# Kernel tuning notes

Hardware: AMD Instinct MI355X
Metric: run time of the kernel (lower is better)

Reference implementation:

```python
import jax, jax.numpy as jnp
import numpy as np

B, L, D = 4, 4096, 1024
H = 4
DK = D // H          # head key dim = 256
DV = D // H          # head value dim = 256
CHUNK = 32
CONV_K = 4
FIR_S, FIR_L = 5, 63
N_PATHS = 4
TAU_MIN = 0.25
HARD_FLOOR = 0.005
LEARN_FLOOR_MAX = 0.07
EPS = 1e-5


def _silu(x):
    return x * jax.nn.sigmoid(x)


def _l2norm(x):
    return x * jax.lax.rsqrt(jnp.sum(x * x, -1, keepdims=True) + 1e-6)


def _causal_dw_conv(x, filt):
    # x: (B, L, C); filt: (C, K). Depthwise causal conv1d.
    C, K = filt.shape
    xp = jnp.pad(x, ((0, 0), (K - 1, 0), (0, 0)))
    w = filt.T[:, None, :]  # (K, 1, C)
    return jax.lax.conv_general_dilated(xp, w, (1,), 'VALID',
                                        dimension_numbers=('NWC', 'WIO', 'NWC'),
                                        feature_group_count=C)


def _fir(x, filt):
    # x: (B, L, H, Dv); filt: (H, Dv, K)
    b, l, h, d = x.shape
    y = _causal_dw_conv(x.reshape(b, l, h * d), filt.reshape(h * d, filt.shape[-1]))
    return y.reshape(b, l, h, d)


def _delta_rule_chunkwise(q, k, v, beta):
    # q,k: (B,H,L,dk); v: (B,H,L,dv); beta: (B,H,L). L must be a multiple of CHUNK.
    b, h, Lq, dk = q.shape
    dv = v.shape[-1]
    q = _l2norm(q)
    k = _l2norm(k)
    v = v * beta[..., None]
    kb = k * beta[..., None]
    n = Lq // CHUNK
    r = lambda t: t.reshape(b, h, n, CHUNK, t.shape[-1])
    q, k, v, kb = r(q), r(k), r(v), r(kb)
    # A = strictly-lower part of -(k_beta @ k^T); the torch row loop computes
    # (I - A)^{-1} - I via forward substitution, then adds I back.
    A = -jnp.einsum('bhnid,bhnjd->bhnij', kb, k)
    A = jnp.tril(A, -1)
    eye = jnp.eye(CHUNK, dtype=q.dtype)
    Tinv = jax.scipy.linalg.solve_triangular(eye - A, jnp.broadcast_to(eye, A.shape),
                                             lower=True, unit_diagonal=True)
    u = Tinv @ v   # (b,h,n,c,dv)
    w = Tinv @ kb  # (b,h,n,c,dk)

    def step(S, inp):
        q_i, k_i, u_i, w_i = inp  # (b,h,c,d)
        attn = jnp.tril(jnp.einsum('bhid,bhjd->bhij', q_i, k_i))  # incl. diagonal
        u_adj = u_i - w_i @ S
        o_i = q_i @ S + attn @ u_adj
        S_new = S + jnp.einsum('bhcd,bhce->bhde', k_i, u_adj)
        return S_new, o_i

    S0 = jnp.zeros((b, h, dk, dv), dtype=q.dtype)
    xs = tuple(jnp.moveaxis(t, 2, 0) for t in (q, k, u, w))
    S, o = jax.lax.scan(step, S0, xs)
    o = jnp.moveaxis(o, 0, 2).reshape(b, h, Lq, dv)
    return o, S


def _stats(p):
    # p: (B,L,H,D) -> (B,L,H*4): mean, var (biased), mean|.|, l2 norm
    mean = p.mean(-1)
    var = p.var(-1)
    absm = jnp.abs(p).mean(-1)
    l2 = jnp.sqrt(jnp.sum(p * p, -1))
    s = jnp.stack([mean, var, absm, l2], -1)
    return s.reshape(p.shape[0], p.shape[1], -1)


def setup_inputs() -> dict:
    key = jax.random.key(0)
    ks = jax.random.split(key, 16)
    rn = lambda i, shape, s=0.02: jax.random.normal(ks[i], shape, jnp.float32) * s
    GATE_IN = D + 16 * H
    GATE_H = D * 2 // 2
    return {
        'hidden_states': jax.random.normal(ks[0], (B, L, D), jnp.float32),
        'Wq': rn(1, (D, D)), 'Wk': rn(2, (D, D)), 'Wv': rn(3, (D, D)),
        'Wb': rn(4, (H, D)),
        'conv_q_w': rn(5, (D, CONV_K), 0.2),
        'conv_k_w': rn(6, (D, CONV_K), 0.2),
        'conv_v_w': rn(7, (D, CONV_K), 0.2),
        'fir_short_w': rn(8, (H, DV, FIR_S)).at[..., -1].add(1.0),
        'fir_long_w': rn(9, (H, DV, FIR_L)).at[..., -1].add(1.0),
        'log_temp': jnp.zeros((H, N_PATHS), jnp.float32),
        'floor_param': jnp.full((H, N_PATHS), -2.0, jnp.float32),
        'gate_W1': rn(10, (GATE_H, GATE_IN)),
        'gate_b1': jnp.zeros((GATE_H,), jnp.float32),
        'gate_W2': rn(11, (H * N_PATHS, GATE_H)),
        'gate_b2': jnp.zeros((H * N_PATHS,), jnp.float32).at[N_PATHS - 1::N_PATHS].set(2.0),
        'o_norm_w': jnp.ones((DV,), jnp.float32),
        'Wo': rn(12, (D, D)),
    }


def reference(hidden_states, Wq, Wk, Wv, Wb, conv_q_w, conv_k_w, conv_v_w,
              fir_short_w, fir_long_w, log_temp, floor_param,
              gate_W1, gate_b1, gate_W2, gate_b2, o_norm_w, Wo):
    b, l, _ = hidden_states.shape
    # projections + short depthwise causal conv with silu activation
    q = _silu(_causal_dw_conv(hidden_states @ Wq.T, conv_q_w))
    k = _silu(_causal_dw_conv(hidden_states @ Wk.T, conv_k_w))
    v = _silu(_causal_dw_conv(hidden_states @ Wv.T, conv_v_w))
    beta = jax.nn.sigmoid(hidden_states @ Wb.T)  # (b,l,H)

    q_h = q.reshape(b, l, H, DK).transpose(0, 2, 1, 3)
    k_h = k.reshape(b, l, H, DK).transpose(0, 2, 1, 3)
    v_h = v.reshape(b, l, H, DV).transpose(0, 2, 1, 3)
    o_d, _S = _delta_rule_chunkwise(q_h, k_h, v_h, beta.transpose(0, 2, 1))
    path_delta = o_d.transpose(0, 2, 1, 3)  # (b,l,H,DV)

    v_direct = v.reshape(b, l, H, DV)
    path_short = _fir(v_direct, fir_short_w)
    path_long = _fir(v_direct, fir_long_w)

    gate_in = jnp.concatenate([hidden_states, _stats(path_short), _stats(path_long),
                               _stats(path_delta), _stats(v_direct)], -1)
    h1 = jax.nn.gelu(gate_in @ gate_W1.T + gate_b1, approximate=False)
    logits = (h1 @ gate_W2.T + gate_b2).reshape(b, l, H, N_PATHS)
    tau = jax.nn.softplus(log_temp) + TAU_MIN  # (H,4)
    probs = jax.nn.softmax(logits / tau, axis=-1)
    floor = jnp.minimum(HARD_FLOOR + jax.nn.sigmoid(floor_param) * LEARN_FLOOR_MAX, 0.25)
    sum_floor = jnp.minimum(jnp.sum(floor, -1, keepdims=True), 0.99)
    norm_floor = floor / sum_floor * 0.99
    clipped = jnp.maximum(probs, norm_floor + 1e-9)
    weights = clipped / (jnp.sum(clipped, -1, keepdims=True) + 1e-8)  # (b,l,H,4)

    paths = jnp.stack([path_short, path_long, path_delta, v_direct], axis=3)  # (b,l,H,4,DV)
    o = jnp.einsum('blhp,blhpd->blhd', weights, paths)
    o = o * jax.lax.rsqrt(jnp.mean(o * o, -1, keepdims=True) + EPS) * o_norm_w  # per-head RMSNorm
    return o.reshape(b, l, H * DV) @ Wo.T
```

## Files before the change

### kernel.cpp

```cpp
#include <hip/hip_runtime.h>
#include <hip/hip_bf16.h>
#include <cstddef>

#define NB 4
#define NL 4096
#define ND 1024
#define NH 4
#define NDK 256
#define NCH 128

typedef __hip_bfloat16 bf16;
typedef __attribute__((ext_vector_type(8))) short bf16x8;
typedef __attribute__((ext_vector_type(4))) float f32x4;

__device__ __forceinline__ float sigf(float x){ return 1.0f/(1.0f + expf(-x)); }
__device__ __forceinline__ float geluf(float x){ return 0.5f*x*(1.0f+erff(x*0.70710678118654752f)); }
__device__ __forceinline__ float us2f(unsigned short s){ return __uint_as_float(((unsigned int)s)<<16); }
__device__ __forceinline__ float b2f(bf16 x){ return __bfloat162float(x); }
__device__ __forceinline__ bf16  f2b(float x){ return __float2bfloat16(x); }
__device__ __forceinline__ unsigned short f2bu(float x){ bf16 h = f2b(x); return *(unsigned short*)&h; }

__device__ __forceinline__ float4 ld4f(const float* p){ return *(const float4*)p; }
__device__ __forceinline__ float4 ld4f(const bf16* p){
    ushort4 u = *(const ushort4*)p;
    return make_float4(us2f(u.x), us2f(u.y), us2f(u.z), us2f(u.w));
}
__device__ __forceinline__ void st4(float* p, float4 v){ *(float4*)p = v; }
__device__ __forceinline__ void st4(bf16* p, float4 v){
    bf16 a=f2b(v.x), b=f2b(v.y), c=f2b(v.z), d=f2b(v.w);
    ushort4 u;
    u.x=*(unsigned short*)&a; u.y=*(unsigned short*)&b;
    u.z=*(unsigned short*)&c; u.w=*(unsigned short*)&d;
    *(ushort4*)p = u;
}

#define DOT4(v, s) ((v).x*(s).x + (v).y*(s).y + (v).z*(s).z + (v).w*(s).w)

template<typename XT, int ACT, typename CT>
__global__ __launch_bounds__(256) void gemm_mfma(const XT* __restrict__ X,
    const float* __restrict__ W, const float* __restrict__ bias,
    CT* __restrict__ C, int M, int N, int K)
{
    constexpr int SX = (sizeof(XT)==4) ? 1 : 0;
    __shared__ unsigned short Ah[128*40];
    __shared__ unsigned short Al[SX ? 128*40 : 8];
    __shared__ unsigned short Bh[128*40];
    __shared__ unsigned short Bl[128*40];
    const int t = threadIdx.x;
    const int wid = t >> 6, l = t & 63;
    const int wr = wid >> 1, wc = wid & 1;
    const int bm = blockIdx.y*128, bn = blockIdx.x*128;
    const int sr = t >> 1, sk = (t & 1)*16;
    const XT* Xb = X + (size_t)(bm+sr)*K + sk;
    const float* Wb = W + (size_t)(bn+sr)*K + sk;
    const int lr = l & 15, lk = (l >> 4)*8;
    f32x4 acc[4][4];
    #pragma unroll
    for (int i=0;i<4;i++)
        #pragma unroll
        for (int j=0;j<4;j++) acc[i][j] = (f32x4){0.f,0.f,0.f,0.f};

    for (int kt = 0; kt < K; kt += 32) {
        unsigned short hx[16], lx[16], hw[16], lw[16];
        {
            float wf[16];
            *(float4*)&wf[0]  = ld4f(Wb + kt);
            *(float4*)&wf[4]  = ld4f(Wb + kt + 4);
            *(float4*)&wf[8]  = ld4f(Wb + kt + 8);
            *(float4*)&wf[12] = ld4f(Wb + kt + 12);
            #pragma unroll
            for (int j=0;j<16;j++){
                bf16 h = f2b(wf[j]);
                hw[j] = *(unsigned short*)&h;
                lw[j] = f2bu(wf[j] - b2f(h));
            }
        }
        if constexpr (SX){
            float xf[16];
            *(float4*)&xf[0]  = ld4f(Xb + kt);
            *(float4*)&xf[4]  = ld4f(Xb + kt + 4);
            *(float4*)&xf[8]  = ld4f(Xb + kt + 8);
            *(float4*)&xf[12] = ld4f(Xb + kt + 12);
            #pragma unroll
            for (int j=0;j<16;j++){
                bf16 h = f2b(xf[j]);
                hx[j] = *(unsigned short*)&h;
                lx[j] = f2bu(xf[j] - b2f(h));
            }
        } else {
            *(uint4*)&hx[0] = *(const uint4*)(Xb + kt);
            *(uint4*)&hx[8] = *(const uint4*)(Xb + kt + 8);
        }
        __syncthreads();
        *(uint4*)&Ah[sr*40 + sk]     = *(uint4*)&hx[0];
        *(uint4*)&Ah[sr*40 + sk + 8] = *(uint4*)&hx[8];
        if constexpr (SX){
            *(uint4*)&Al[sr*40 + sk]     = *(uint4*)&lx[0];
            *(uint4*)&Al[sr*40 + sk + 8] = *(uint4*)&lx[8];
        }
        *(uint4*)&Bh[sr*40 + sk]     = *(uint4*)&hw[0];
        *(uint4*)&Bh[sr*40 + sk + 8] = *(uint4*)&hw[8];
        *(uint4*)&Bl[sr*40 + sk]     = *(uint4*)&lw[0];
        *(uint4*)&Bl[sr*40 + sk + 8] = *(uint4*)&lw[8];
        __syncthreads();
        bf16x8 ah[4], al[4];
        #pragma unroll
        for (int mi=0;mi<4;mi++){
            ah[mi] = *(const bf16x8*)&Ah[(wr*64 + mi*16 + lr)*40 + lk];
            if constexpr (SX) al[mi] = *(const bf16x8*)&Al[(wr*64 + mi*16 + lr)*40 + lk];
        }
        #pragma unroll
        for (int nj=0;nj<4;nj++){
            bf16x8 bh = *(const bf16x8*)&Bh[(wc*64 + nj*16 + lr)*40 + lk];
            bf16x8 bl = *(const bf16x8*)&Bl[(wc*64 + nj*16 + lr)*40 + lk];
            #pragma unroll
            for (int mi=0;mi<4;mi++){
                acc[mi][nj] = __builtin_amdgcn_mfma_f32_16x16x32_bf16(ah[mi], bh, acc[mi][nj], 0,0,0);
                acc[mi][nj] = __builtin_amdgcn_mfma_f32_16x16x32_bf16(ah[mi], bl, acc[mi][nj], 0,0,0);
                if constexpr (SX)
                    acc[mi][nj] = __builtin_amdgcn_mfma_f32_16x16x32_bf16(al[mi], bh, acc[mi][nj], 0,0,0);
            }
        }
    }
    const int cr0 = (l >> 4) * 4;
    #pragma unroll
    for (int nj=0;nj<4;nj++){
        const int col = bn + wc*64 + nj*16 + lr;
        const float bv = bias ? bias[col] : 0.f;
        #pragma unroll
        for (int mi=0;mi<4;mi++){
            const int m0 = bm + wr*64 + mi*16 + cr0;
            #pragma unroll
            for (int r=0;r<4;r++){
                float v = acc[mi][nj][r] + bv;
                if (ACT==1) v = geluf(v);
                if constexpr (sizeof(CT)==2) C[(size_t)(m0+r)*N + col] = f2b(v);
                else                         C[(size_t)(m0+r)*N + col] = v;
            }
        }
    }
}

__global__ __launch_bounds__(256) void ftrans_kernel(const float* __restrict__ f,
    float* __restrict__ ft, int K)
{
    int idx = blockIdx.x*256 + threadIdx.x;
    if (idx < ND*K){
        int c = idx / K, k = idx - c*K;
        ft[k*ND + c] = f[idx];
    }
}

template<int K, int ACT>
__global__ __launch_bounds__(256) void dwconv3_kernel(const bf16* __restrict__ x,
    const float* __restrict__ ft, bf16* __restrict__ y)
{
    const int tr = threadIdx.x >> 7;
    const int c8 = (threadIdx.x & 127) * 8;
    const long row0 = (long)blockIdx.x * 16 + tr * 8;
    const int l0 = (int)(row0 & (NL - 1));
    const long bbase = row0 - l0;
    float xw[8][8];
    float acc[8][8];
    #pragma unroll
    for (int r=0;r<8;r++)
        #pragma unroll
        for (int j=0;j<8;j++) acc[r][j] = 0.f;
    #pragma unroll
    for (int w2=0;w2<8;w2++){
        int ls = l0 - (K-1) + w2;
        if (ls >= 0){
            const bf16* p = x + (bbase + ls)*ND + c8;
            ushort4 lo = *(const ushort4*)p;
            ushort4 hi = *(const ushort4*)(p + 4);
            xw[w2][0]=us2f(lo.x); xw[w2][1]=us2f(lo.y); xw[w2][2]=us2f(lo.z); xw[w2][3]=us2f(lo.w);
            xw[w2][4]=us2f(hi.x); xw[w2][5]=us2f(hi.y); xw[w2][6]=us2f(hi.z); xw[w2][7]=us2f(hi.w);
        } else {
            #pragma unroll
            for (int j=0;j<8;j++) xw[w2][j]=0.f;
        }
    }
    #pragma unroll
    for (int tt=0;tt<K;tt++){
        float4 f0 = *(const float4*)(ft + (size_t)tt*ND + c8);
        float4 f1 = *(const float4*)(ft + (size_t)tt*ND + c8 + 4);
        float fv[8] = {f0.x,f0.y,f0.z,f0.w,f1.x,f1.y,f1.z,f1.w};
        #pragma unroll
        for (int r=0;r<8;r++){
            const int sl = (tt + r) & 7;
            #pragma unroll
            for (int j=0;j<8;j++) acc[r][j] += xw[sl][j]*fv[j];
        }
        if (tt < K-1){
            const int sl = tt & 7;
            int ls = l0 - (K-1) + tt + 8;
            if (ls >= 0){
                const bf16* p = x + (bbase + ls)*ND + c8;
                ushort4 lo = *(const ushort4*)p;
                ushort4 hi = *(const ushort4*)(p + 4);
                xw[sl][0]=us2f(lo.x); xw[sl][1]=us2f(lo.y); xw[sl][2]=us2f(lo.z); xw[sl][3]=us2f(lo.w);
                xw[sl][4]=us2f(hi.x); xw[sl][5]=us2f(hi.y); xw[sl][6]=us2f(hi.z); xw[sl][7]=us2f(hi.w);
            } else {
                #pragma unroll
                for (int j=0;j<8;j++) xw[sl][j]=0.f;
            }
        }
    }
    #pragma unroll
    for (int r=0;r<8;r++){
        bf16* yp = y + (bbase + l0 + r)*ND + c8;
        float o[8];
        #pragma unroll
        for (int j=0;j<8;j++){
            float v = acc[r][j];
            if (ACT) v = v * sigf(v);
            o[j] = v;
        }
        st4(yp,   make_float4(o[0],o[1],o[2],o[3]));
        st4(yp+4, make_float4(o[4],o[5],o[6],o[7]));
    }
}

__global__ __launch_bounds__(256) void beta_kernel(const float* __restrict__ hs,
    const float* __restrict__ Wb, float* __restrict__ beta)
{
    const int wid = (int)((blockIdx.x*256 + threadIdx.x) >> 6);
    const int lane = threadIdx.x & 63;
    const int h = wid & 3, row = wid >> 2;
    const float* x = hs + (size_t)row*ND;
    const float* w = Wb + (size_t)h*ND;
    float s = 0.f;
    for (int i = lane; i < ND; i += 64) s += x[i]*w[i];
    #pragma unroll
    for (int o=32;o>0;o>>=1) s += __shfl_xor(s,o);
    if (lane == 0) beta[(size_t)row*NH + h] = sigf(s);
}

__global__ __launch_bounds__(256) void prep_kernel(bf16* __restrict__ q, bf16* __restrict__ k)
{
    const int row = blockIdx.x;
    const int h = threadIdx.x >> 6, lane = threadIdx.x & 63;
    const size_t off = (size_t)row*ND + h*NDK + lane*4;
    float4 q4 = ld4f(q + off);
    float4 k4 = ld4f(k + off);
    float sq = q4.x*q4.x+q4.y*q4.y+q4.z*q4.z+q4.w*q4.w;
    float sk = k4.x*k4.x+k4.y*k4.y+k4.z*k4.z+k4.w*k4.w;
    #pragma unroll
    for (int o=32;o>0;o>>=1){ sq += __shfl_xor(sq,o); sk += __shfl_xor(sk,o); }
    float rq = rsqrtf(sq + 1e-6f), rk = rsqrtf(sk + 1e-6f);
    q4.x*=rq; q4.y*=rq; q4.z*=rq; q4.w*=rq;
    k4.x*=rk; k4.y*=rk; k4.z*=rk; k4.w*=rk;
    st4(q + off, q4);
    st4(k + off, k4);
}

__global__ __launch_bounds__(256) void ut_kernel(const bf16* __restrict__ qn,
    const bf16* __restrict__ kn, const bf16* __restrict__ vv,
    const float* __restrict__ beta, bf16* __restrict__ u_,
    bf16* __restrict__ w_, bf16* __restrict__ attn)
{
    __shared__ float ks[32][257];
    __shared__ float qs[32][257];
    __shared__ float dkk[32][33];
    __shared__ float Ti[32][33];
    __shared__ float bs[32];
    const int blk = blockIdx.x;
    const int n = blk & (NCH-1), bh = blk >> 7;
    const int b = bh >> 2, h = bh & 3;
    const int t = threadIdx.x;
    const size_t base = ((size_t)b*NL + n*32)*ND + h*NDK;
    #pragma unroll
    for (int r=0;r<8;r++){
        int idx = t + (r<<8);
        int i = idx >> 6, dp = (idx & 63) << 2;
        float4 kv = ld4f(kn + base + (size_t)i*ND + dp);
        ks[i][dp]=kv.x; ks[i][dp+1]=kv.y; ks[i][dp+2]=kv.z; ks[i][dp+3]=kv.w;
        float4 qv = ld4f(qn + base + (size_t)i*ND + dp);
        qs[i][dp]=qv.x; qs[i][dp+1]=qv.y; qs[i][dp+2]=qv.z; qs[i][dp+3]=qv.w;
    }
    if (t < 32) bs[t] = beta[((size_t)b*NL + n*32 + t)*NH + h];
    __syncthreads();
    #pragma unroll
    for (int p=0;p<4;p++){
        const int i = (t>>5) + (p<<3), j = t & 31;
        float aK=0.f, aA=0.f;
        for (int d2=0; d2<256; d2++){
            float kj = ks[j][d2];
            aK += ks[i][d2]*kj;
            aA += qs[i][d2]*kj;
        }
        dkk[i][j] = aK;
        attn[((size_t)bh*NCH + n)*1024 + i*32 + j] = f2b((j<=i)? aA : 0.f);
    }
    __syncthreads();
    if (t < 32) Ti[0][t] = (t==0)?1.f:0.f;
    __syncthreads();
    for (int i=1;i<32;i++){
        if (t < 32){
            const int j = t;
            float v;
            if (j > i) v = 0.f;
            else if (j == i) v = 1.f;
            else {
                float acc = 0.f;
                for (int p2=j;p2<i;p2++) acc += dkk[i][p2]*Ti[p2][j];
                v = -bs[i]*acc;
            }
            Ti[i][j] = v;
        }
        __syncthreads();
    }
    {
        float ua[32];
        #pragma unroll
        for (int i=0;i<32;i++) ua[i]=0.f;
        for (int j=0;j<32;j++){
            float vj = b2f(vv[base + (size_t)j*ND + t]) * bs[j];
            #pragma unroll
            for (int i=0;i<32;i++) ua[i] += Ti[i][j]*vj;
        }
        #pragma unroll
        for (int i=0;i<32;i++) u_[base + (size_t)i*ND + t] = f2b(ua[i]);
        #pragma unroll
        for (int i=0;i<32;i++) ua[i]=0.f;
        for (int j=0;j<32;j++){
            float kjv = ks[j][t]*bs[j];
            #pragma unroll
            for (int i=0;i<32;i++) ua[i] += Ti[i][j]*kjv;
        }
        #pragma unroll
        for (int i=0;i<32;i++) w_[base + (size_t)i*ND + t] = f2b(ua[i]);
    }
}

__global__ __launch_bounds__(256) void scan8_kernel(const bf16* __restrict__ qn,
    const bf16* __restrict__ kn, const bf16* __restrict__ u_,
    const bf16* __restrict__ w_, const bf16* __restrict__ attn,
    bf16* __restrict__ pd)
{
    __shared__ unsigned short bw[32][268];
    __shared__ unsigned short bq[32][268];
    __shared__ unsigned short bk[32][268];
    __shared__ float St[8][260];
    __shared__ float ual[32][12];
    __shared__ float atl[32][33];
    const int blk = blockIdx.x;
    const int sl = blk >> 4;
    const int bh = blk & 15;
    const int b = bh >> 2, h = bh & 3;
    const int d0 = sl * 8;
    const int t = threadIdx.x;
    const int li = t & 31, dg = t >> 5;
    const int cg = t & 63, dh = t >> 6;
    for (int i = t; i < 8*260; i += 256) ((float*)St)[i] = 0.f;
    const bf16* qb = qn + (size_t)b*NL*ND + h*NDK;
    const bf16* kb = kn + (size_t)b*NL*ND + h*NDK;
    const bf16* ub = u_ + (size_t)b*NL*ND + h*NDK;
    const bf16* wb = w_ + (size_t)b*NL*ND + h*NDK;
    const bf16* ab = attn + (size_t)bh*NCH*1024;
    bf16* pdb = pd + (size_t)b*NL*ND + h*NDK + d0;
    for (int n=0;n<NCH;n++){
        const size_t cb = (size_t)n*32*ND;
        __syncthreads();
        #pragma unroll
        for (int it=0;it<8;++it){
            int idx = it*256 + t;
            int row = idx >> 6, c4 = (idx & 63)*4;
            *(ushort4*)&bw[row][c4] = *(const ushort4*)&wb[cb + (size_t)row*ND + c4];
            *(ushort4*)&bq[row][c4] = *(const ushort4*)&qb[cb + (size_t)row*ND + c4];
            *(ushort4*)&bk[row][c4] = *(const ushort4*)&kb[cb + (size_t)row*ND + c4];
        }
        #pragma unroll
        for (int r=0;r<4;r++){ int idx = t + (r<<8); atl[idx>>5][idx&31] = b2f(ab[(size_t)n*1024 + idx]); }
        __syncthreads();
        float uaAcc = b2f(ub[cb + (size_t)li*ND + d0 + dg]);
        float oAcc = 0.f;
        for (int cgi=0; cgi<64; cgi++){
            ushort4 wv4 = *(const ushort4*)&bw[li][cgi*4];
            ushort4 qv4 = *(const ushort4*)&bq[li][cgi*4];
            float4 wv = make_float4(us2f(wv4.x),us2f(wv4.y),us2f(wv4.z),us2f(wv4.w));
            float4 qv = make_float4(us2f(qv4.x),us2f(qv4.y),us2f(qv4.z),us2f(qv4.w));
            float4 s = *(const float4*)&St[dg][cgi*4];
            uaAcc -= DOT4(wv, s);
            oAcc  += DOT4(qv, s);
        }
        ual[li][dg] = uaAcc;
        __syncthreads();
        for (int j=0;j<32;j++) oAcc += atl[li][j]*ual[j][dg];
        pdb[(size_t)(n*32 + li)*ND + dg] = f2b(oAcc);
        float4 sac0 = make_float4(0.f,0.f,0.f,0.f);
        float4 sac1 = make_float4(0.f,0.f,0.f,0.f);
        for (int j=0;j<32;j++){
            ushort4 kv4 = *(const ushort4*)&bk[j][cg*4];
            float4 kv = make_float4(us2f(kv4.x),us2f(kv4.y),us2f(kv4.z),us2f(kv4.w));
            float u0 = ual[j][dh*2];
            float u1 = ual[j][dh*2+1];
            sac0.x += kv.x*u0; sac0.y += kv.y*u0; sac0.z += kv.z*u0; sac0.w += kv.w*u0;
            sac1.x += kv.x*u1; sac1.y += kv.y*u1; sac1.z += kv.z*u1; sac1.w += kv.w*u1;
        }
        {
            float4* sp0 = (float4*)&St[dh*2+0][cg*4];
            float4 c0 = *sp0;
            c0.x += sac0.x; c0.y += sac0.y; c0.z += sac0.z; c0.w += sac0.w;
            *sp0 = c0;
            float4* sp1 = (float4*)&St[dh*2+1][cg*4];
            float4 c1 = *sp1;
            c1.x += sac1.x; c1.y += sac1.y; c1.z += sac1.z; c1.w += sac1.w;
            *sp1 = c1;
        }
    }
}

__global__ __launch_bounds__(256) void gate_in_kernel(const float* __restrict__ hs,
    const bf16* __restrict__ ps, const bf16* __restrict__ pl,
    const bf16* __restrict__ pdl, const bf16* __restrict__ vc,
    bf16* __restrict__ gin)
{
    const int row = blockIdx.x;
    const int t = threadIdx.x;
    const int h = t >> 6, lane = t & 63;
    float4 hv = ld4f(hs + (size_t)row*ND + t*4);
    st4(gin + (size_t)row*1088 + t*4, hv);
    const size_t off = (size_t)row*ND + h*NDK + lane*4;
    const bf16* srcs[4] = {ps, pl, pdl, vc};
    #pragma unroll
    for (int p=0;p<4;p++){
        float4 v = ld4f(srcs[p] + off);
        float sx = v.x+v.y+v.z+v.w;
        float sq = v.x*v.x+v.y*v.y+v.z*v.z+v.w*v.w;
        float sa = fabsf(v.x)+fabsf(v.y)+fabsf(v.z)+fabsf(v.w);
        #pragma unroll
        for (int o=32;o>0;o>>=1){ sx+=__shfl_xor(sx,o); sq+=__shfl_xor(sq,o); sa+=__shfl_xor(sa,o); }
        if (lane==0){
            float mean = sx*(1.f/256.f);
            float var  = sq*(1.f/256.f) - mean*mean;
            bf16* o2 = gin + (size_t)row*1088 + 1024 + p*16 + h*4;
            o2[0]=f2b(mean); o2[1]=f2b(var); o2[2]=f2b(sa*(1.f/256.f)); o2[3]=f2b(sqrtf(sq));
        }
    }
}

__global__ __launch_bounds__(256) void gate_weights_kernel(const bf16* __restrict__ h1,
    const float* __restrict__ W2, const float* __restrict__ b2,
    const float* __restrict__ log_temp, const float* __restrict__ fp,
    float* __restrict__ wt)
{
    __shared__ float part[16][17];
    __shared__ float lg[16];
    const int row = blockIdx.x, t = threadIdx.x;
    const int o = t >> 4, g = t & 15;
    const bf16* hr = h1 + (size_t)row*1024;
    const float* wr = W2 + (size_t)o*1024;
    float s = 0.f;
    for (int i2=0;i2<64;i2++){ int k = g + (i2<<4); s += b2f(hr[k])*wr[k]; }
    part[o][g] = s;
    __syncthreads();
    if (t < 16){
        float acc = b2[t];
        #pragma unroll
        for (int g2=0;g2<16;g2++) acc += part[t][g2];
        lg[t] = acc;
    }
    __syncthreads();
    if (t < 4){
        const int h = t;
        float x[4], fl[4];
        float mx = -1e30f;
        #pragma unroll
        for (int p=0;p<4;p++){
            float lt = log_temp[h*4+p];
            float tau = (lt > 20.f ? lt : log1pf(expf(lt))) + 0.25f;
            x[p] = lg[h*4+p] / tau;
            mx = fmaxf(mx, x[p]);
        }
        float se = 0.f;
        #pragma unroll
        for (int p=0;p<4;p++){ x[p] = expf(x[p]-mx); se += x[p]; }
        float sfl = 0.f;
        #pragma unroll
        for (int p=0;p<4;p++){
            fl[p] = fminf(0.005f + sigf(fp[h*4+p])*0.07f, 0.25f);
            sfl += fl[p];
        }
        float sf = fminf(sfl, 0.99f);
        float cs = 0.f;
        float cl[4];
        #pragma unroll
        for (int p=0;p<4;p++){
            float prob = x[p]/se;
            float nf = fl[p]/sf*0.99f;
            cl[p] = fmaxf(prob, nf + 1e-9f);
            cs += cl[p];
        }
        float inv = 1.f/(cs + 1e-8f);
        #pragma unroll
        for (int p=0;p<4;p++) wt[(size_t)row*16 + h*4 + p] = cl[p]*inv;
    }
}

__global__ __launch_bounds__(256) void mix_kernel(const float* wt,
    const bf16* ps, const bf16* pl, const bf16* pdl, const bf16* vc,
    const float* onw, bf16* om)
{
    const int row = blockIdx.x, t = threadIdx.x;
    const int h = t >> 6, lane = t & 63;
    const size_t off = (size_t)row*ND + h*NDK + lane*4;
    const float w0 = wt[(size_t)row*16+h*4+0];
    const float w1 = wt[(size_t)row*16+h*4+1];
    const float w2 = wt[(size_t)row*16+h*4+2];
    const float w3 = wt[(size_t)row*16+h*4+3];
    float4 a = ld4f(ps+off);
    float4 b4 = ld4f(pl+off);
    float4 c = ld4f(pdl+off);
    float4 d = ld4f(vc+off);
    float4 o;
    o.x = w0*a.x + w1*b4.x + w2*c.x + w3*d.x;
    o.y = w0*a.y + w1*b4.y + w2*c.y + w3*d.y;
    o.z = w0*a.z + w1*b4.z + w2*c.z + w3*d.z;
    o.w = w0*a.w + w1*b4.w + w2*c.w + w3*d.w;
    float sq = o.x*o.x+o.y*o.y+o.z*o.z+o.w*o.w;
    #pragma unroll
    for (int oo=32;oo>0;oo>>=1) sq += __shfl_xor(sq,oo);
    float r = rsqrtf(sq*(1.f/256.f) + 1e-5f);
    float4 nw = *(const float4*)(onw + lane*4);
    o.x *= r*nw.x; o.y *= r*nw.y; o.z *= r*nw.z; o.w *= r*nw.w;
    st4(om+off, o);
}

extern "C" void kernel_launch(void* const* d_in, const int* in_sizes, int n_in,
                              void* d_out, int out_size, void* d_ws, size_t ws_size,
                              hipStream_t stream)
{
    const float* hs  = (const float*)d_in[0];
    const float* Wq  = (const float*)d_in[1];
    const float* Wk  = (const float*)d_in[2];
    const float* Wv  = (const float*)d_in[3];
    const float* Wbp = (const float*)d_in[4];
    const float* cq  = (const float*)d_in[5];
    const float* ck  = (const float*)d_in[6];
    const float* cv  = (const float*)d_in[7];
    const float* fsw = (const float*)d_in[8];
    const float* flw = (const float*)d_in[9];
    const float* log_temp = (const float*)d_in[10];
    const float* floor_p  = (const float*)d_in[11];
    const float* gW1 = (const float*)d_in[12];
    const float* gb1 = (const float*)d_in[13];
    const float* gW2 = (const float*)d_in[14];
    const float* gb2 = (const float*)d_in[15];
    const float* onw = (const float*)d_in[16];
    const float* Wo  = (const float*)d_in[17];

    const size_t NEEDED = 206831616ULL;
    if (ws_size < NEEDED) return;

    const size_t E = 16777216ULL;
    bf16* W = (bf16*)d_ws;
    bf16* B0 = W;
    bf16* B1 = W + E;
    bf16* B2 = W + 2*E;
    bf16* B3 = W + 3*E;
    bf16* B4 = W + 4*E;
    bf16* B5 = W + 5*E;
    bf16* attnb = W + 6*E;
    bf16* gin = B4;
    bf16* h1  = B4 + 17825792;
    float* beta = (float*)((char*)d_ws + 205520896);
    float* wt   = (float*)((char*)d_ws + 205783040);
    float* ftc = (float*)attnb;
    float* fts = (float*)attnb;
    float* ftl = (float*)attnb + 8192;

    dim3 gg(8, 128);
    gemm_mfma<float,0,bf16><<<gg,256,0,stream>>>(hs, Wq, nullptr, B0, 16384, 1024, 1024);
    ftrans_kernel<<<16,256,0,stream>>>(cq, ftc, 4);
    dwconv3_kernel<4,1><<<1024,256,0,stream>>>(B0, ftc, B1);
    gemm_mfma<float,0,bf16><<<gg,256,0,stream>>>(hs, Wk, nullptr, B0, 16384, 1024, 1024);
    ftrans_kernel<<<16,256,0,stream>>>(ck, ftc, 4);
    dwconv3_kernel<4,1><<<1024,256,0,stream>>>(B0, ftc, B2);
    gemm_mfma<float,0,bf16><<<gg,256,0,stream>>>(hs, Wv, nullptr, B0, 16384, 1024, 1024);
    ftrans_kernel<<<16,256,0,stream>>>(cv, ftc, 4);
    dwconv3_kernel<4,1><<<1024,256,0,stream>>>(B0, ftc, B3);
    beta_kernel<<<16384,256,0,stream>>>(hs, Wbp, beta);
    prep_kernel<<<16384,256,0,stream>>>(B1, B2);
    ut_kernel<<<2048,256,0,stream>>>(B1, B2, B3, beta, B4, B5, attnb);
    scan8_kernel<<<512,256,0,stream>>>(B1, B2, B4, B5, attnb, B0);
    ftrans_kernel<<<20,256,0,stream>>>(fsw, fts, 5);
    dwconv3_kernel<5,0><<<1024,256,0,stream>>>(B3, fts, B1);
    ftrans_kernel<<<252,256,0,stream>>>(flw, ftl, 63);
    dwconv3_kernel<63,0><<<1024,256,0,stream>>>(B3, ftl, B2);
    gate_in_kernel<<<16384,256,0,stream>>>(hs, B1, B2, B0, B3, gin);
    gemm_mfma<bf16,1,bf16><<<gg,256,0,stream>>>(gin, gW1, gb1, h1, 16384, 1024, 1088);
    gate_weights_kernel<<<16384,256,0,stream>>>(h1, gW2, gb2, log_temp, floor_p, wt);
    mix_kernel<<<16384,256,0,stream>>>(wt, B1, B2, B0, B3, onw, B3);
    gemm_mfma<bf16,0,float><<<gg,256,0,stream>>>(B3, Wo, nullptr, (float*)d_out, 16384, 1024, 1024);
}
```

Before: 2.783 ms.

## Widen delta-rule scan blocks to 16 value columns with split-K partial sums

The chunkwise delta-rule scan now gives each block 16 value columns instead of 8, using 512 threads and half as many blocks. The two thread halves each reduce half of the key dimension, and their partial sums are combined through shared memory before the intra-chunk attention and the state update. Each chunk's q, k and w tiles are loaded once per 16 value columns rather than once per 8, which halves redundant global loads. The cost is one extra barrier per chunk, more shared memory per block, and only 256 blocks to fill the GPU.

```diff
diff --git a/kernel.cpp b/kernel.cpp
--- a/kernel.cpp
+++ b/kernel.cpp
@@ -333,7 +333,7 @@
     }
 }
 
-__global__ __launch_bounds__(256) void scan8_kernel(const bf16* __restrict__ qn,
+__global__ __launch_bounds__(512) void scan16c_kernel(const bf16* __restrict__ qn,
     const bf16* __restrict__ kn, const bf16* __restrict__ u_,
     const bf16* __restrict__ w_, const bf16* __restrict__ attn,
     bf16* __restrict__ pd)
@@ -341,18 +341,23 @@
     __shared__ unsigned short bw[32][268];
     __shared__ unsigned short bq[32][268];
     __shared__ unsigned short bk[32][268];
-    __shared__ float St[8][260];
-    __shared__ float ual[32][12];
+    __shared__ float St[16][260];
+    __shared__ float ual[32][21];
+    __shared__ float uap[2][32][21];
+    __shared__ float oap[2][32][21];
     __shared__ float atl[32][33];
     const int blk = blockIdx.x;
     const int sl = blk >> 4;
     const int bh = blk & 15;
     const int b = bh >> 2, h = bh & 3;
-    const int d0 = sl * 8;
+    const int d0 = sl * 16;
     const int t = threadIdx.x;
-    const int li = t & 31, dg = t >> 5;
+    const int half = t >> 8;
+    const int tt = t & 255;
+    const int li = tt & 31, dg = tt >> 5;
+    const int r1 = t >> 4, c1 = t & 15;
     const int cg = t & 63, dh = t >> 6;
-    for (int i = t; i < 8*260; i += 256) ((float*)St)[i] = 0.f;
+    for (int i = t; i < 16*260; i += 512) ((float*)St)[i] = 0.f;
     const bf16* qb = qn + (size_t)b*NL*ND + h*NDK;
     const bf16* kb = kn + (size_t)b*NL*ND + h*NDK;
     const bf16* ub = u_ + (size_t)b*NL*ND + h*NDK;
@@ -363,31 +368,43 @@
         const size_t cb = (size_t)n*32*ND;
         __syncthreads();
         #pragma unroll
-        for (int it=0;it<8;++it){
-            int idx = it*256 + t;
+        for (int it=0;it<4;++it){
+            int idx = it*512 + t;
             int row = idx >> 6, c4 = (idx & 63)*4;
             *(ushort4*)&bw[row][c4] = *(const ushort4*)&wb[cb + (size_t)row*ND + c4];
             *(ushort4*)&bq[row][c4] = *(const ushort4*)&qb[cb + (size_t)row*ND + c4];
             *(ushort4*)&bk[row][c4] = *(const ushort4*)&kb[cb + (size_t)row*ND + c4];
         }
         #pragma unroll
-        for (int r=0;r<4;r++){ int idx = t + (r<<8); atl[idx>>5][idx&31] = b2f(ab[(size_t)n*1024 + idx]); }
+        for (int r=0;r<2;r++){ int idx = t + (r<<9); atl[idx>>5][idx&31] = b2f(ab[(size_t)n*1024 + idx]); }
         __syncthreads();
-        float uaAcc = b2f(ub[cb + (size_t)li*ND + d0 + dg]);
-        float oAcc = 0.f;
-        for (int cgi=0; cgi<64; cgi++){
+        float ua0 = 0.f, ua1 = 0.f, o0 = 0.f, o1 = 0.f;
+        if (half == 0){
+            ua0 = b2f(ub[cb + (size_t)li*ND + d0 + dg*2]);
+            ua1 = b2f(ub[cb + (size_t)li*ND + d0 + dg*2 + 1]);
+        }
+        const int cbase = half*32;
+        for (int ci=0; ci<32; ci++){
+            const int cgi = cbase + ci;
             ushort4 wv4 = *(const ushort4*)&bw[li][cgi*4];
             ushort4 qv4 = *(const ushort4*)&bq[li][cgi*4];
             float4 wv = make_float4(us2f(wv4.x),us2f(wv4.y),us2f(wv4.z),us2f(wv4.w));
             float4 qv = make_float4(us2f(qv4.x),us2f(qv4.y),us2f(qv4.z),us2f(qv4.w));
-            float4 s = *(const float4*)&St[dg][cgi*4];
-            uaAcc -= DOT4(wv, s);
-            oAcc  += DOT4(qv, s);
-        }
-        ual[li][dg] = uaAcc;
+            float4 s0 = *(const float4*)&St[dg*2+0][cgi*4];
+            float4 s1 = *(const float4*)&St[dg*2+1][cgi*4];
+            ua0 -= DOT4(wv, s0);  ua1 -= DOT4(wv, s1);
+            o0  += DOT4(qv, s0);  o1  += DOT4(qv, s1);
+        }
+        uap[half][li][dg*2]   = ua0;
+        uap[half][li][dg*2+1] = ua1;
+        oap[half][li][dg*2]   = o0;
+        oap[half][li][dg*2+1] = o1;
         __syncthreads();
-        for (int j=0;j<32;j++) oAcc += atl[li][j]*ual[j][dg];
-        pdb[(size_t)(n*32 + li)*ND + dg] = f2b(oAcc);
+        float oc = oap[0][r1][c1] + oap[1][r1][c1];
+        ual[r1][c1] = uap[0][r1][c1] + uap[1][r1][c1];
+        __syncthreads();
+        for (int j=0;j<32;j++) oc += atl[r1][j]*ual[j][c1];
+        pdb[(size_t)(n*32 + r1)*ND + c1] = f2b(oc);
         float4 sac0 = make_float4(0.f,0.f,0.f,0.f);
         float4 sac1 = make_float4(0.f,0.f,0.f,0.f);
         for (int j=0;j<32;j++){
@@ -404,9 +421,9 @@
             c0.x += sac0.x; c0.y += sac0.y; c0.z += sac0.z; c0.w += sac0.w;
             *sp0 = c0;
             float4* sp1 = (float4*)&St[dh*2+1][cg*4];
-            float4 c1 = *sp1;
-            c1.x += sac1.x; c1.y += sac1.y; c1.z += sac1.z; c1.w += sac1.w;
-            *sp1 = c1;
+            float4 cc1 = *sp1;
+            cc1.x += sac1.x; cc1.y += sac1.y; cc1.z += sac1.z; cc1.w += sac1.w;
+            *sp1 = cc1;
         }
     }
 }
@@ -583,7 +600,7 @@
     beta_kernel<<<16384,256,0,stream>>>(hs, Wbp, beta);
     prep_kernel<<<16384,256,0,stream>>>(B1, B2);
     ut_kernel<<<2048,256,0,stream>>>(B1, B2, B3, beta, B4, B5, attnb);
-    scan8_kernel<<<512,256,0,stream>>>(B1, B2, B4, B5, attnb, B0);
+    scan16c_kernel<<<256,512,0,stream>>>(B1, B2, B4, B5, attnb, B0);
     ftrans_kernel<<<20,256,0,stream>>>(fsw, fts, 5);
     dwconv3_kernel<5,0><<<1024,256,0,stream>>>(B3, fts, B1);
     ftrans_kernel<<<252,256,0,stream>>>(flw, ftl, 63);
```

Result: faster. 2.642 ms (-5.1%).

## Widen scan blocks to 16 value columns and stage chunk tiles as fp32

Applied to the files above, without the earlier changes.

The delta-rule scan kernel now assigns 16 value columns per block with 512 threads, halving the block count to 256. Each block reuses its staged q/k/w chunk tiles across twice as many state columns. Those tiles are converted from bf16 to fp32 once during staging instead of inside every inner-loop read. This cuts redundant global loads and conversion work per block. The cost is roughly double the shared memory footprint and fewer blocks, which lowers parallelism on a GPU with many compute units.

```diff
diff --git a/kernel.cpp b/kernel.cpp
--- a/kernel.cpp
+++ b/kernel.cpp
@@ -333,26 +333,26 @@
     }
 }
 
-__global__ __launch_bounds__(256) void scan8_kernel(const bf16* __restrict__ qn,
+__global__ __launch_bounds__(512) void scan16e_kernel(const bf16* __restrict__ qn,
     const bf16* __restrict__ kn, const bf16* __restrict__ u_,
     const bf16* __restrict__ w_, const bf16* __restrict__ attn,
     bf16* __restrict__ pd)
 {
-    __shared__ unsigned short bw[32][268];
-    __shared__ unsigned short bq[32][268];
-    __shared__ unsigned short bk[32][268];
-    __shared__ float St[8][260];
-    __shared__ float ual[32][12];
+    __shared__ float bwf[32][258];
+    __shared__ float bqf[32][258];
+    __shared__ float bkf[32][258];
+    __shared__ float St[16][260];
+    __shared__ float ual[32][21];
     __shared__ float atl[32][33];
     const int blk = blockIdx.x;
     const int sl = blk >> 4;
     const int bh = blk & 15;
     const int b = bh >> 2, h = bh & 3;
-    const int d0 = sl * 8;
+    const int d0 = sl * 16;
     const int t = threadIdx.x;
     const int li = t & 31, dg = t >> 5;
     const int cg = t & 63, dh = t >> 6;
-    for (int i = t; i < 8*260; i += 256) ((float*)St)[i] = 0.f;
+    for (int i = t; i < 16*260; i += 512) ((float*)St)[i] = 0.f;
     const bf16* qb = qn + (size_t)b*NL*ND + h*NDK;
     const bf16* kb = kn + (size_t)b*NL*ND + h*NDK;
     const bf16* ub = u_ + (size_t)b*NL*ND + h*NDK;
@@ -363,36 +363,36 @@
         const size_t cb = (size_t)n*32*ND;
         __syncthreads();
         #pragma unroll
-        for (int it=0;it<8;++it){
-            int idx = it*256 + t;
+        for (int it=0;it<4;++it){
+            int idx = it*512 + t;
             int row = idx >> 6, c4 = (idx & 63)*4;
-            *(ushort4*)&bw[row][c4] = *(const ushort4*)&wb[cb + (size_t)row*ND + c4];
-            *(ushort4*)&bq[row][c4] = *(const ushort4*)&qb[cb + (size_t)row*ND + c4];
-            *(ushort4*)&bk[row][c4] = *(const ushort4*)&kb[cb + (size_t)row*ND + c4];
-        }
-        #pragma unroll
-        for (int r=0;r<4;r++){ int idx = t + (r<<8); atl[idx>>5][idx&31] = b2f(ab[(size_t)n*1024 + idx]); }
+            ushort4 wv = *(const ushort4*)&wb[cb + (size_t)row*ND + c4];
+            *(float4*)&bwf[row][c4] = make_float4(us2f(wv.x),us2f(wv.y),us2f(wv.z),us2f(wv.w));
+            ushort4 qv = *(const ushort4*)&qb[cb + (size_t)row*ND + c4];
+            *(float4*)&bqf[row][c4] = make_float4(us2f(qv.x),us2f(qv.y),us2f(qv.z),us2f(qv.w));
+            ushort4 kv = *(const ushort4*)&kb[cb + (size_t)row*ND + c4];
+            *(float4*)&bkf[row][c4] = make_float4(us2f(kv.x),us2f(kv.y),us2f(kv.z),us2f(kv.w));
+        }
+        #pragma unroll
+        for (int r=0;r<2;r++){ int idx = t + (r<<9); atl[idx>>5][idx&31] = b2f(ab[(size_t)n*1024 + idx]); }
         __syncthreads();
-        float uaAcc = b2f(ub[cb + (size_t)li*ND + d0 + dg]);
-        float oAcc = 0.f;
+        float ua = b2f(ub[cb + (size_t)li*ND + d0 + dg]);
+        float o = 0.f;
         for (int cgi=0; cgi<64; cgi++){
-            ushort4 wv4 = *(const ushort4*)&bw[li][cgi*4];
-            ushort4 qv4 = *(const ushort4*)&bq[li][cgi*4];
-            float4 wv = make_float4(us2f(wv4.x),us2f(wv4.y),us2f(wv4.z),us2f(wv4.w));
-            float4 qv = make_float4(us2f(qv4.x),us2f(qv4.y),us2f(qv4.z),us2f(qv4.w));
-            float4 s = *(const float4*)&St[dg][cgi*4];
-            uaAcc -= DOT4(wv, s);
-            oAcc  += DOT4(qv, s);
-        }
-        ual[li][dg] = uaAcc;
+            float4 wv = *(const float4*)&bwf[li][cgi*4];
+            float4 qv = *(const float4*)&bqf[li][cgi*4];
+            float4 s  = *(const float4*)&St[dg][cgi*4];
+            ua -= DOT4(wv, s);
+            o  += DOT4(qv, s);
+        }
+        ual[li][dg] = ua;
         __syncthreads();
-        for (int j=0;j<32;j++) oAcc += atl[li][j]*ual[j][dg];
-        pdb[(size_t)(n*32 + li)*ND + dg] = f2b(oAcc);
+        for (int j=0;j<32;j++) o += atl[li][j]*ual[j][dg];
+        pdb[(size_t)(n*32 + li)*ND + dg] = f2b(o);
         float4 sac0 = make_float4(0.f,0.f,0.f,0.f);
         float4 sac1 = make_float4(0.f,0.f,0.f,0.f);
         for (int j=0;j<32;j++){
-            ushort4 kv4 = *(const ushort4*)&bk[j][cg*4];
-            float4 kv = make_float4(us2f(kv4.x),us2f(kv4.y),us2f(kv4.z),us2f(kv4.w));
+            float4 kv = *(const float4*)&bkf[j][cg*4];
             float u0 = ual[j][dh*2];
             float u1 = ual[j][dh*2+1];
             sac0.x += kv.x*u0; sac0.y += kv.y*u0; sac0.z += kv.z*u0; sac0.w += kv.w*u0;
@@ -404,9 +404,9 @@
             c0.x += sac0.x; c0.y += sac0.y; c0.z += sac0.z; c0.w += sac0.w;
             *sp0 = c0;
             float4* sp1 = (float4*)&St[dh*2+1][cg*4];
-            float4 c1 = *sp1;
-            c1.x += sac1.x; c1.y += sac1.y; c1.z += sac1.z; c1.w += sac1.w;
-            *sp1 = c1;
+            float4 cc1 = *sp1;
+            cc1.x += sac1.x; cc1.y += sac1.y; cc1.z += sac1.z; cc1.w += sac1.w;
+            *sp1 = cc1;
         }
     }
 }
@@ -583,7 +583,7 @@
     beta_kernel<<<16384,256,0,stream>>>(hs, Wbp, beta);
     prep_kernel<<<16384,256,0,stream>>>(B1, B2);
     ut_kernel<<<2048,256,0,stream>>>(B1, B2, B3, beta, B4, B5, attnb);
-    scan8_kernel<<<512,256,0,stream>>>(B1, B2, B4, B5, attnb, B0);
+    scan16e_kernel<<<256,512,0,stream>>>(B1, B2, B4, B5, attnb, B0);
     ftrans_kernel<<<20,256,0,stream>>>(fsw, fts, 5);
     dwconv3_kernel<5,0><<<1024,256,0,stream>>>(B3, fts, B1);
     ftrans_kernel<<<252,256,0,stream>>>(flw, ftl, 63);
```

Result: slower. 3.012 ms (+8.2%).
